# Kernel tuning notes

Measured on AMD Instinct MI355X. Metric: run time of the kernel, lower is better.

The kernel has to match this reference:

```python
import jax, jax.numpy as jnp
import numpy as np

EPS = 1e-6
N, D = 8192, 256


def setup_inputs() -> dict:
    key = jax.random.key(0)
    kq, kc = jax.random.split(key)
    # scale 0.05 keeps points inside the Poincare ball: c*||q||^2 ~ 0.06 << 1
    query = jax.random.normal(kq, (N, D), dtype=jnp.float32) * 0.05
    c = jnp.asarray(0.1, dtype=jnp.float32)  # learnable curvature param (init 0.1)
    return {"query": query, "c": c}


def reference(query, c):
    # Self-attention path of HyperbolicAttention (keys = values = query).
    clamp_c = jnp.maximum(c, EPS)
    # ||u-v||^2 = ||u||^2 + ||v||^2 - 2 u.v  (same math as explicit expand+subtract,
    # but via a single GEMM instead of an (N, N, D) intermediate)
    qn = jnp.sum(query * query, axis=-1)                       # (N,)
    gram = query @ query.T                                     # (N, N)
    diff_sq = jnp.maximum(qn[:, None] + qn[None, :] - 2.0 * gram, 0.0)
    t = jnp.maximum(1.0 - clamp_c * qn, EPS)                   # clamped 1 - c||x||^2
    denom = t[:, None] * t[None, :]                            # (N, N)
    arg = jnp.maximum(1.0 + 2.0 * clamp_c * diff_sq / denom, 1.0 + EPS) + EPS
    dist = jnp.arccosh(arg) / jnp.sqrt(clamp_c)                # (N, N)
    attn = jax.nn.softmax(-dist, axis=-1)                      # (N, N)
    return attn @ query                                        # (N, D)
```

## Files before the change

kernel.cpp:

```cpp
#include <hip/hip_runtime.h>
#include <math.h>

#define NN 8192
#define DD 256
#define EPSV 1e-6f
#define BM 64
#define BN 64
#define CSPLIT 4
#define COLS_PER_BLOCK (NN / CSPLIT)
#define NJT (COLS_PER_BLOCK / BN)
#define PSTR 72
#define SMEM_BYTES (32768 + 32768 + BM * PSTR * 2)

typedef __bf16 bf16x8 __attribute__((ext_vector_type(8)));
typedef float f32x16 __attribute__((ext_vector_type(16)));
typedef unsigned short ushort;
typedef unsigned int uint;


__device__ inline ushort f2bf(float x) {
    uint u = __float_as_uint(x);
    u += 0x7fffu + ((u >> 16) & 1u);
    return (ushort)(u >> 16);
}

__device__ inline void gload_lds16(const void* g, void* l) {
    __builtin_amdgcn_global_load_lds((const __attribute__((address_space(1))) uint*)g,
                                     (__attribute__((address_space(3))) uint*)l, 16, 0, 0);
}

__global__ void zero_kernel(float* __restrict__ p) {
    int i = blockIdx.x * 256 + threadIdx.x;
    ((float4*)p)[i] = make_float4(0.f, 0.f, 0.f, 0.f);
}

__global__ void cvt_kernel(const float* __restrict__ q, ushort* __restrict__ qbf) {
    int g = blockIdx.x * 256 + threadIdx.x;
    int r = g >> 5, c = g & 31;
    const float4* src = (const float4*)(q + (size_t)r * DD + c * 8);
    float4 v0 = src[0], v1 = src[1];
    ushort o[8] = {f2bf(v0.x), f2bf(v0.y), f2bf(v0.z), f2bf(v0.w),
                   f2bf(v1.x), f2bf(v1.y), f2bf(v1.z), f2bf(v1.w)};
    *(uint4*)(qbf + (size_t)r * DD + ((c ^ (r & 7)) * 8)) = *(uint4*)o;
}

__global__ void tr_kernel(const float* __restrict__ q, ushort* __restrict__ qbfT) {
    __shared__ ushort T[64 * PSTR];
    int p0 = blockIdx.x * 64, f0 = blockIdx.y * 64;
    int t = threadIdx.x;
    int pr = t >> 2, fs = (t & 3) * 16;
    const float4* src = (const float4*)(q + (size_t)(p0 + pr) * DD + f0 + fs);
    #pragma unroll
    for (int i = 0; i < 4; ++i) {
        float4 v = src[i];
        ushort o[4] = {f2bf(v.x), f2bf(v.y), f2bf(v.z), f2bf(v.w)};
        *(ushort4*)&T[pr * PSTR + fs + i * 4] = *(ushort4*)o;
    }
    __syncthreads();
    int fr = t >> 2;
    int f = f0 + fr;
    #pragma unroll
    for (int half = 0; half < 2; ++half) {
        int cgpos = (t & 3) * 2 + half;
        int cg = cgpos ^ (f & 7);
        ushort tmp[8];
        #pragma unroll
        for (int j = 0; j < 8; ++j) tmp[j] = T[(cg * 8 + j) * PSTR + fr];
        *(uint4*)(qbfT + (size_t)f * NN + p0 + cgpos * 8) = *(uint4*)tmp;
    }
}

__global__ void qn_kernel(const float* __restrict__ q, const float* __restrict__ cp,
                          float* __restrict__ qn, float* __restrict__ itv) {
    int row = blockIdx.x * 4 + (threadIdx.x >> 6);
    int lane = threadIdx.x & 63;
    float4 v = ((const float4*)(q + (size_t)row * DD))[lane];
    float a = __uint_as_float((uint)f2bf(v.x) << 16);
    float b = __uint_as_float((uint)f2bf(v.y) << 16);
    float c2 = __uint_as_float((uint)f2bf(v.z) << 16);
    float d = __uint_as_float((uint)f2bf(v.w) << 16);
    float s = a * a + b * b + c2 * c2 + d * d;
    #pragma unroll
    for (int off = 32; off; off >>= 1) s += __shfl_xor(s, off, 64);
    if (lane == 0) {
        float cc = fmaxf(cp[0], EPSV);
        qn[row] = s;
        float tt = fmaxf(1.0f - cc * s, EPSV);
        itv[row] = 1.0f / tt;
    }
}

__global__ __launch_bounds__(256, 2) void flash_kernel(
    const ushort* __restrict__ qbf, const ushort* __restrict__ qbfT,
    const float* __restrict__ cp, const float* __restrict__ qn,
    const float* __restrict__ itv, float* __restrict__ Oacc, float* __restrict__ lacc) {
    extern __shared__ char smem[];
    ushort* Klds = (ushort*)smem;
    ushort* Ktlds = (ushort*)(smem + 32768);
    ushort* Plds = (ushort*)(smem + 65536);

    const int tid = threadIdx.x;
    const int lane = tid & 63;
    const int w = tid >> 6;
    const int l31 = lane & 31;
    const int lhi = lane >> 5;
    const int qr = w >> 1;
    const int qc = w & 1;
    const int R0 = blockIdx.y * BM;
    const int C0 = blockIdx.x * COLS_PER_BLOCK;

    const float cc = fmaxf(cp[0], EPSV);
    const float rsc = rsqrtf(cc);
    const float k2c = 2.0f * cc;

    const int rowA = R0 + qr * 32 + l31;
    const ushort* qrow = qbf + (size_t)rowA * DD;
    bf16x8 qa[16];
    #pragma unroll
    for (int kk = 0; kk < 16; ++kk) {
        int c = kk * 2 + lhi;
        qa[kk] = *(const bf16x8*)(qrow + ((c ^ (rowA & 7)) * 8));
    }

    float qnr16[16], itr16[16];
    #pragma unroll
    for (int r = 0; r < 16; ++r) {
        int row = R0 + qr * 32 + (r & 3) + 8 * (r >> 2) + 4 * lhi;
        qnr16[r] = qn[row];
        itr16[r] = itv[row];
    }

    f32x16 o[4];
    #pragma unroll
    for (int ct = 0; ct < 4; ++ct)
        #pragma unroll
        for (int i = 0; i < 16; ++i) o[ct][i] = 0.f;
    float rsum = 0.f;

    {
        const char* gbase = (const char*)(qbf + (size_t)C0 * DD);
        #pragma unroll
        for (int i = 0; i < 8; ++i) {
            int chunk = w * 8 + i;
            gload_lds16(gbase + chunk * 1024 + lane * 16, (char*)Klds + chunk * 1024);
        }
    }

    for (int jt = 0; jt < NJT; ++jt) {
        const int C = C0 + jt * BN;
        __syncthreads();

        {
            int fr = lane >> 3, cg = lane & 7;
            #pragma unroll
            for (int i = 0; i < 8; ++i) {
                int f0 = w * 64 + i * 8;
                gload_lds16((const char*)(qbfT + (size_t)(f0 + fr) * NN + C) + cg * 16,
                            (char*)Ktlds + f0 * 128 + lane * 16);
            }
        }

        f32x16 s;
        #pragma unroll
        for (int i = 0; i < 16; ++i) s[i] = 0.f;
        const int jrow = qc * 32 + l31;
        const ushort* krow = Klds + jrow * DD;
        #pragma unroll
        for (int kk = 0; kk < 16; ++kk) {
            int c = kk * 2 + lhi;
            bf16x8 b = *(const bf16x8*)(krow + ((c ^ (jrow & 7)) * 8));
            s = __builtin_amdgcn_mfma_f32_32x32x16_bf16(qa[kk], b, s, 0, 0, 0);
        }

        {
            int J = C + jrow;
            float qnj = qn[J];
            float itj = itv[J];
            #pragma unroll
            for (int r = 0; r < 16; ++r) {
                int mloc = qr * 32 + (r & 3) + 8 * (r >> 2) + 4 * lhi;
                float diff = fmaxf(qnr16[r] + qnj - 2.0f * s[r], 0.0f);
                float u = k2c * diff * itr16[r] * itj;
                float arg = fmaxf(1.0f + u, 1.0f + EPSV) + EPSV;
                float y = arg + sqrtf((arg - 1.0f) * (arg + 1.0f));
                float p = __builtin_amdgcn_exp2f(-rsc * __builtin_amdgcn_logf(y));
                Plds[mloc * PSTR + jrow] = f2bf(p);
            }
        }
        __syncthreads();

        if (jt + 1 < NJT) {
            const char* gbase = (const char*)(qbf + (size_t)(C + BN) * DD);
            #pragma unroll
            for (int i = 0; i < 8; ++i) {
                int chunk = w * 8 + i;
                gload_lds16(gbase + chunk * 1024 + lane * 16, (char*)Klds + chunk * 1024);
            }
        }

        {
            const ushort* prow = Plds + (tid >> 2) * PSTR + (tid & 3) * 16;
            uint4 a = *(const uint4*)prow;
            uint4 b = *(const uint4*)(prow + 8);
            uint ua[8] = {a.x, a.y, a.z, a.w, b.x, b.y, b.z, b.w};
            float ssum = 0.f;
            #pragma unroll
            for (int i = 0; i < 8; ++i) {
                ssum += __uint_as_float(ua[i] << 16);
                ssum += __uint_as_float(ua[i] & 0xffff0000u);
            }
            rsum += ssum;
        }

        #pragma unroll
        for (int kt = 0; kt < 4; ++kt) {
            bf16x8 pa = *(const bf16x8*)&Plds[(qr * 32 + l31) * PSTR + kt * 16 + 8 * lhi];
            #pragma unroll
            for (int ct = 0; ct < 4; ++ct) {
                int drow = qc * 128 + ct * 32 + l31;
                int cch = kt * 2 + lhi;
                bf16x8 vb = *(const bf16x8*)(Ktlds + drow * 64 + ((cch ^ (drow & 7)) * 8));
                o[ct] = __builtin_amdgcn_mfma_f32_32x32x16_bf16(pa, vb, o[ct], 0, 0, 0);
            }
        }
    }

    #pragma unroll
    for (int ct = 0; ct < 4; ++ct) {
        #pragma unroll
        for (int r = 0; r < 16; ++r) {
            int row = R0 + qr * 32 + (r & 3) + 8 * (r >> 2) + 4 * lhi;
            int d = qc * 128 + ct * 32 + l31;
            atomicAdd(&Oacc[(size_t)row * DD + d], o[ct][r]);
        }
    }
    float tot = rsum;
    tot += __shfl_xor(tot, 1, 64);
    tot += __shfl_xor(tot, 2, 64);
    if ((tid & 3) == 0) atomicAdd(&lacc[R0 + (tid >> 2)], tot);
}

__global__ void norm_kernel(const float* __restrict__ Oacc, const float* __restrict__ lacc,
                            float* __restrict__ out) {
    int i = blockIdx.x * 256 + threadIdx.x;
    float4 v = ((const float4*)Oacc)[i];
    float inv = 1.0f / lacc[i >> 6];
    ((float4*)out)[i] = make_float4(v.x * inv, v.y * inv, v.z * inv, v.w * inv);
}

extern "C" void kernel_launch(void* const* d_in, const int* in_sizes, int n_in,
                              void* d_out, int out_size, void* d_ws, size_t ws_size,
                              hipStream_t stream) {
    (void)in_sizes; (void)n_in; (void)out_size; (void)ws_size;
    const float* q = (const float*)d_in[0];
    const float* cp = (const float*)d_in[1];
    float* out = (float*)d_out;
    float* ws = (float*)d_ws;
    float* Oacc = ws;
    float* lacc = ws + (size_t)NN * DD;
    float* qn = lacc + NN;
    float* itv = qn + NN;
    ushort* qbf = (ushort*)(itv + NN);
    ushort* qbfT = qbf + (size_t)NN * DD;

    static int smem_set = 0;
    if (!smem_set) {
        hipFuncSetAttribute((const void*)flash_kernel,
                            hipFuncAttributeMaxDynamicSharedMemorySize, SMEM_BYTES);
        smem_set = 1;
    }

    zero_kernel<<<(NN * DD + NN) / 4 / 256, 256, 0, stream>>>(ws);
    cvt_kernel<<<NN * DD / 8 / 256, 256, 0, stream>>>(q, qbf);
    tr_kernel<<<dim3(NN / 64, DD / 64), 256, 0, stream>>>(q, qbfT);
    qn_kernel<<<NN / 4, 256, 0, stream>>>(q, cp, qn, itv);
    flash_kernel<<<dim3(CSPLIT, NN / BM), 256, SMEM_BYTES, stream>>>(qbf, qbfT, cp, qn, itv, Oacc, lacc);
    norm_kernel<<<(NN * DD / 4) / 256, 256, 0, stream>>>(Oacc, lacc, out);
}
```

Baseline: 209.7 us.

## Fuse prep kernels and load V fragments directly from global memory

Merges the bf16 conversion, transpose and norm kernels into a single prep kernel, and folds sqrt(2c) into the precomputed inverse term. In the flash kernel the V tile no longer goes through LDS: each lane loads its MFMA operand fragments directly from the transposed global array, double-buffered in registers. Row sums are now accumulated from fp32 probabilities in registers rather than re-read from LDS, and LDS use drops to about 41 KB of static shared memory. The cost is uncoalesced, latency-exposed global loads per kt step and extra VGPR pressure. Row sums also now use unrounded fp32 probabilities rather than the bf16 values fed to the MFMA.

Result: slower. 284.3 us (+35.6%).

```diff
diff --git a/kernel.cpp b/kernel.cpp
--- a/kernel.cpp
+++ b/kernel.cpp
@@ -10,7 +10,7 @@
 #define COLS_PER_BLOCK (NN / CSPLIT)
 #define NJT (COLS_PER_BLOCK / BN)
 #define PSTR 72
-#define SMEM_BYTES (32768 + 32768 + BM * PSTR * 2)
+#define TSTR 266
 
 typedef __bf16 bf16x8 __attribute__((ext_vector_type(8)));
 typedef float f32x16 __attribute__((ext_vector_type(16)));
@@ -34,70 +34,59 @@
     ((float4*)p)[i] = make_float4(0.f, 0.f, 0.f, 0.f);
 }
 
-__global__ void cvt_kernel(const float* __restrict__ q, ushort* __restrict__ qbf) {
-    int g = blockIdx.x * 256 + threadIdx.x;
-    int r = g >> 5, c = g & 31;
-    const float4* src = (const float4*)(q + (size_t)r * DD + c * 8);
-    float4 v0 = src[0], v1 = src[1];
-    ushort o[8] = {f2bf(v0.x), f2bf(v0.y), f2bf(v0.z), f2bf(v0.w),
-                   f2bf(v1.x), f2bf(v1.y), f2bf(v1.z), f2bf(v1.w)};
-    *(uint4*)(qbf + (size_t)r * DD + ((c ^ (r & 7)) * 8)) = *(uint4*)o;
-}
-
-__global__ void tr_kernel(const float* __restrict__ q, ushort* __restrict__ qbfT) {
-    __shared__ ushort T[64 * PSTR];
-    int p0 = blockIdx.x * 64, f0 = blockIdx.y * 64;
-    int t = threadIdx.x;
-    int pr = t >> 2, fs = (t & 3) * 16;
-    const float4* src = (const float4*)(q + (size_t)(p0 + pr) * DD + f0 + fs);
-    #pragma unroll
-    for (int i = 0; i < 4; ++i) {
+__global__ void prep_kernel(const float* __restrict__ q, const float* __restrict__ cp,
+                            ushort* __restrict__ qbf, ushort* __restrict__ qbfT,
+                            float* __restrict__ qn, float* __restrict__ itv2) {
+    __shared__ ushort T[64 * TSTR];
+    const int t = threadIdx.x;
+    const int p0 = blockIdx.x * 64;
+    const int pr = t >> 2, fq = t & 3;
+    const int row = p0 + pr;
+    const float4* src = (const float4*)(q + (size_t)row * DD + fq * 64);
+    ushort loc[64];
+    float ss = 0.f;
+    #pragma unroll
+    for (int i = 0; i < 16; ++i) {
         float4 v = src[i];
-        ushort o[4] = {f2bf(v.x), f2bf(v.y), f2bf(v.z), f2bf(v.w)};
-        *(ushort4*)&T[pr * PSTR + fs + i * 4] = *(ushort4*)o;
+        ushort b0 = f2bf(v.x), b1 = f2bf(v.y), b2 = f2bf(v.z), b3 = f2bf(v.w);
+        loc[i * 4 + 0] = b0; loc[i * 4 + 1] = b1; loc[i * 4 + 2] = b2; loc[i * 4 + 3] = b3;
+        float r0 = __uint_as_float((uint)b0 << 16), r1 = __uint_as_float((uint)b1 << 16);
+        float r2 = __uint_as_float((uint)b2 << 16), r3 = __uint_as_float((uint)b3 << 16);
+        ss += r0 * r0 + r1 * r1 + r2 * r2 + r3 * r3;
+    }
+    #pragma unroll
+    for (int k = 0; k < 8; ++k)
+        *(uint4*)(qbf + (size_t)row * DD + (((fq * 8 + k) ^ (row & 7)) * 8)) = *(uint4*)&loc[k * 8];
+    #pragma unroll
+    for (int k = 0; k < 32; ++k)
+        *(ushort2*)&T[pr * TSTR + fq * 64 + k * 2] = *(ushort2*)&loc[k * 2];
+    ss += __shfl_xor(ss, 1, 64);
+    ss += __shfl_xor(ss, 2, 64);
+    if (fq == 0) {
+        float cc = fmaxf(cp[0], EPSV);
+        qn[row] = ss;
+        float tt = fmaxf(1.0f - cc * ss, EPSV);
+        itv2[row] = sqrtf(2.0f * cc) / tt;
     }
     __syncthreads();
-    int fr = t >> 2;
-    int f = f0 + fr;
-    #pragma unroll
-    for (int half = 0; half < 2; ++half) {
-        int cgpos = (t & 3) * 2 + half;
-        int cg = cgpos ^ (f & 7);
-        ushort tmp[8];
-        #pragma unroll
-        for (int j = 0; j < 8; ++j) tmp[j] = T[(cg * 8 + j) * PSTR + fr];
-        *(uint4*)(qbfT + (size_t)f * NN + p0 + cgpos * 8) = *(uint4*)tmp;
-    }
-}
-
-__global__ void qn_kernel(const float* __restrict__ q, const float* __restrict__ cp,
-                          float* __restrict__ qn, float* __restrict__ itv) {
-    int row = blockIdx.x * 4 + (threadIdx.x >> 6);
-    int lane = threadIdx.x & 63;
-    float4 v = ((const float4*)(q + (size_t)row * DD))[lane];
-    float a = __uint_as_float((uint)f2bf(v.x) << 16);
-    float b = __uint_as_float((uint)f2bf(v.y) << 16);
-    float c2 = __uint_as_float((uint)f2bf(v.z) << 16);
-    float d = __uint_as_float((uint)f2bf(v.w) << 16);
-    float s = a * a + b * b + c2 * c2 + d * d;
-    #pragma unroll
-    for (int off = 32; off; off >>= 1) s += __shfl_xor(s, off, 64);
-    if (lane == 0) {
-        float cc = fmaxf(cp[0], EPSV);
-        qn[row] = s;
-        float tt = fmaxf(1.0f - cc * s, EPSV);
-        itv[row] = 1.0f / tt;
+    #pragma unroll
+    for (int pass = 0; pass < 4; ++pass) {
+        int f = pass * 64 + (t >> 2);
+        int quarter = t & 3;
+        ushort tmp[16];
+        #pragma unroll
+        for (int i = 0; i < 16; ++i) tmp[i] = T[(quarter * 16 + i) * TSTR + f];
+        *(uint4*)(qbfT + (size_t)f * NN + p0 + quarter * 16) = *(uint4*)&tmp[0];
+        *(uint4*)(qbfT + (size_t)f * NN + p0 + quarter * 16 + 8) = *(uint4*)&tmp[8];
     }
 }
 
 __global__ __launch_bounds__(256, 2) void flash_kernel(
     const ushort* __restrict__ qbf, const ushort* __restrict__ qbfT,
     const float* __restrict__ cp, const float* __restrict__ qn,
-    const float* __restrict__ itv, float* __restrict__ Oacc, float* __restrict__ lacc) {
-    extern __shared__ char smem[];
-    ushort* Klds = (ushort*)smem;
-    ushort* Ktlds = (ushort*)(smem + 32768);
-    ushort* Plds = (ushort*)(smem + 65536);
+    const float* __restrict__ itv2, float* __restrict__ Oacc, float* __restrict__ lacc) {
+    __shared__ ushort Klds[64 * 256];
+    __shared__ ushort Plds[64 * PSTR];
 
     const int tid = threadIdx.x;
     const int lane = tid & 63;
@@ -111,7 +100,6 @@
 
     const float cc = fmaxf(cp[0], EPSV);
     const float rsc = rsqrtf(cc);
-    const float k2c = 2.0f * cc;
 
     const int rowA = R0 + qr * 32 + l31;
     const ushort* qrow = qbf + (size_t)rowA * DD;
@@ -127,7 +115,7 @@
     for (int r = 0; r < 16; ++r) {
         int row = R0 + qr * 32 + (r & 3) + 8 * (r >> 2) + 4 * lhi;
         qnr16[r] = qn[row];
-        itr16[r] = itv[row];
+        itr16[r] = itv2[row];
     }
 
     f32x16 o[4];
@@ -135,7 +123,14 @@
     for (int ct = 0; ct < 4; ++ct)
         #pragma unroll
         for (int i = 0; i < 16; ++i) o[ct][i] = 0.f;
-    float rsum = 0.f;
+    float racc[16];
+    #pragma unroll
+    for (int r = 0; r < 16; ++r) racc[r] = 0.f;
+
+    const ushort* vbase[4];
+    #pragma unroll
+    for (int ct = 0; ct < 4; ++ct)
+        vbase[ct] = qbfT + (size_t)(qc * 128 + ct * 32 + l31) * NN + 8 * lhi;
 
     {
         const char* gbase = (const char*)(qbf + (size_t)C0 * DD);
@@ -149,16 +144,6 @@
     for (int jt = 0; jt < NJT; ++jt) {
         const int C = C0 + jt * BN;
         __syncthreads();
-
-        {
-            int fr = lane >> 3, cg = lane & 7;
-            #pragma unroll
-            for (int i = 0; i < 8; ++i) {
-                int f0 = w * 64 + i * 8;
-                gload_lds16((const char*)(qbfT + (size_t)(f0 + fr) * NN + C) + cg * 16,
-                            (char*)Ktlds + f0 * 128 + lane * 16);
-            }
-        }
 
         f32x16 s;
         #pragma unroll
@@ -175,18 +160,24 @@
         {
             int J = C + jrow;
             float qnj = qn[J];
-            float itj = itv[J];
+            float itj = itv2[J];
             #pragma unroll
             for (int r = 0; r < 16; ++r) {
                 int mloc = qr * 32 + (r & 3) + 8 * (r >> 2) + 4 * lhi;
                 float diff = fmaxf(qnr16[r] + qnj - 2.0f * s[r], 0.0f);
-                float u = k2c * diff * itr16[r] * itj;
-                float arg = fmaxf(1.0f + u, 1.0f + EPSV) + EPSV;
-                float y = arg + sqrtf((arg - 1.0f) * (arg + 1.0f));
+                float u = diff * itr16[r] * itj;
+                float z = fmaxf(1.0f + u, 1.0f + EPSV) + EPSV;
+                float y = z + sqrtf(fmaf(z, z, -1.0f));
                 float p = __builtin_amdgcn_exp2f(-rsc * __builtin_amdgcn_logf(y));
+                racc[r] += p;
                 Plds[mloc * PSTR + jrow] = f2bf(p);
             }
         }
+
+        bf16x8 vb0[4];
+        #pragma unroll
+        for (int ct = 0; ct < 4; ++ct) vb0[ct] = *(const bf16x8*)(vbase[ct] + C);
+
         __syncthreads();
 
         if (jt + 1 < NJT) {
@@ -198,30 +189,22 @@
             }
         }
 
-        {
-            const ushort* prow = Plds + (tid >> 2) * PSTR + (tid & 3) * 16;
-            uint4 a = *(const uint4*)prow;
-            uint4 b = *(const uint4*)(prow + 8);
-            uint ua[8] = {a.x, a.y, a.z, a.w, b.x, b.y, b.z, b.w};
-            float ssum = 0.f;
-            #pragma unroll
-            for (int i = 0; i < 8; ++i) {
-                ssum += __uint_as_float(ua[i] << 16);
-                ssum += __uint_as_float(ua[i] & 0xffff0000u);
+        bf16x8 cur[4], nxt[4];
+        #pragma unroll
+        for (int ct = 0; ct < 4; ++ct) cur[ct] = vb0[ct];
+        #pragma unroll
+        for (int kt = 0; kt < 4; ++kt) {
+            if (kt < 3) {
+                #pragma unroll
+                for (int ct = 0; ct < 4; ++ct)
+                    nxt[ct] = *(const bf16x8*)(vbase[ct] + C + (kt + 1) * 16);
             }
-            rsum += ssum;
-        }
-
-        #pragma unroll
-        for (int kt = 0; kt < 4; ++kt) {
             bf16x8 pa = *(const bf16x8*)&Plds[(qr * 32 + l31) * PSTR + kt * 16 + 8 * lhi];
             #pragma unroll
-            for (int ct = 0; ct < 4; ++ct) {
-                int drow = qc * 128 + ct * 32 + l31;
-                int cch = kt * 2 + lhi;
-                bf16x8 vb = *(const bf16x8*)(Ktlds + drow * 64 + ((cch ^ (drow & 7)) * 8));
-                o[ct] = __builtin_amdgcn_mfma_f32_32x32x16_bf16(pa, vb, o[ct], 0, 0, 0);
-            }
+            for (int ct = 0; ct < 4; ++ct)
+                o[ct] = __builtin_amdgcn_mfma_f32_32x32x16_bf16(pa, cur[ct], o[ct], 0, 0, 0);
+            #pragma unroll
+            for (int ct = 0; ct < 4; ++ct) cur[ct] = nxt[ct];
         }
     }
 
@@ -234,10 +217,17 @@
             atomicAdd(&Oacc[(size_t)row * DD + d], o[ct][r]);
         }
     }
-    float tot = rsum;
-    tot += __shfl_xor(tot, 1, 64);
-    tot += __shfl_xor(tot, 2, 64);
-    if ((tid & 3) == 0) atomicAdd(&lacc[R0 + (tid >> 2)], tot);
+    #pragma unroll
+    for (int off = 1; off <= 16; off <<= 1)
+        #pragma unroll
+        for (int r = 0; r < 16; ++r) racc[r] += __shfl_xor(racc[r], off, 64);
+    if (l31 == 0) {
+        #pragma unroll
+        for (int r = 0; r < 16; ++r) {
+            int row = R0 + qr * 32 + (r & 3) + 8 * (r >> 2) + 4 * lhi;
+            atomicAdd(&lacc[row], racc[r]);
+        }
+    }
 }
 
 __global__ void norm_kernel(const float* __restrict__ Oacc, const float* __restrict__ lacc,
@@ -259,21 +249,12 @@
     float* Oacc = ws;
     float* lacc = ws + (size_t)NN * DD;
     float* qn = lacc + NN;
-    float* itv = qn + NN;
-    ushort* qbf = (ushort*)(itv + NN);
+    float* itv2 = qn + NN;
+    ushort* qbf = (ushort*)(itv2 + NN);
     ushort* qbfT = qbf + (size_t)NN * DD;
 
-    static int smem_set = 0;
-    if (!smem_set) {
-        hipFuncSetAttribute((const void*)flash_kernel,
-                            hipFuncAttributeMaxDynamicSharedMemorySize, SMEM_BYTES);
-        smem_set = 1;
-    }
-
     zero_kernel<<<(NN * DD + NN) / 4 / 256, 256, 0, stream>>>(ws);
-    cvt_kernel<<<NN * DD / 8 / 256, 256, 0, stream>>>(q, qbf);
-    tr_kernel<<<dim3(NN / 64, DD / 64), 256, 0, stream>>>(q, qbfT);
-    qn_kernel<<<NN / 4, 256, 0, stream>>>(q, cp, qn, itv);
-    flash_kernel<<<dim3(CSPLIT, NN / BM), 256, SMEM_BYTES, stream>>>(qbf, qbfT, cp, qn, itv, Oacc, lacc);
+    prep_kernel<<<NN / 64, 256, 0, stream>>>(q, cp, qbf, qbfT, qn, itv2);
+    flash_kernel<<<dim3(CSPLIT, NN / BM), 256, 0, stream>>>(qbf, qbfT, cp, qn, itv2, Oacc, lacc);
     norm_kernel<<<(NN * DD / 4) / 256, 256, 0, stream>>>(Oacc, lacc, out);
 }
```
